# Kernel tuning notes

Hardware: AMD Instinct MI355X
Metric: run time of the kernel (lower is better)

## Reference

```python
import math
import jax, jax.numpy as jnp
import numpy as np

NUM_CLASSES = 80
CONF_THR = 0.05
IOU_THR = 0.5
MAX_PER_CLASS = 100
MAX_DET = 100
PRE_NMS_K = 200  # per-class candidates kept before greedy NMS (>= max_per_class)
BOX_VAR = np.array([0.1, 0.1, 0.2, 0.2], np.float32)
IMG_H, IMG_W = 640, 640
BATCH = 8


def _anchor_dims():
    ratios = [0.5, 1.0, 2.0]
    scales = [2.0 ** x for x in (0.0, 1.0 / 3.0, 2.0 / 3.0)]
    dims_all = []
    for area in [32.0 ** 2, 64.0 ** 2, 128.0 ** 2, 256.0 ** 2, 512.0 ** 2]:
        dims = []
        for r in ratios:  # ratio-major, scale-minor (matches AnchorBox._compute_dims)
            h = math.sqrt(area / r)
            w = area / h
            for s in scales:
                dims.append([s * w, s * h])
        dims_all.append(np.array(dims, np.float32))  # [9, 2]
    return dims_all


def get_anchors(H, W):
    """Anchors in [cx, cy, w, h], shape [total_anchors, 4] (static, numpy)."""
    strides = [8, 16, 32, 64, 128]
    out = []
    for stride, dims in zip(strides, _anchor_dims()):
        fh, fw = math.ceil(H / stride), math.ceil(W / stride)
        rx = (np.arange(fw, dtype=np.float32) + 0.5) * stride
        ry = (np.arange(fh, dtype=np.float32) + 0.5) * stride
        cx, cy = np.meshgrid(rx, ry)  # each [fh, fw], 'xy' indexing like tf.meshgrid
        centers = np.broadcast_to(np.stack([cx, cy], -1)[:, :, None, :], (fh, fw, 9, 2))
        d = np.broadcast_to(dims[None, None], (fh, fw, 9, 2))
        out.append(np.concatenate([centers, d], -1).reshape(-1, 4))
    return jnp.asarray(np.concatenate(out, 0))


def decode_boxes(anchors, box_pred):
    """Apply variance scaling + anchor offsets, return corner boxes."""
    b = box_pred * jnp.asarray(BOX_VAR)
    xy = b[..., :2] * anchors[..., 2:] + anchors[..., :2]
    wh = jnp.exp(b[..., 2:]) * anchors[..., 2:]
    return jnp.concatenate([xy - wh * 0.5, xy + wh * 0.5], axis=-1)


def pairwise_iou(b):
    lt = jnp.maximum(b[:, None, :2], b[None, :, :2])
    rb = jnp.minimum(b[:, None, 2:], b[None, :, 2:])
    wh = jnp.maximum(rb - lt, 0.0)
    inter = wh[..., 0] * wh[..., 1]
    area = (b[:, 2] - b[:, 0]) * (b[:, 3] - b[:, 1])
    return inter / (area[:, None] + area[None, :] - inter + 1e-8)


def nms_one_class(boxes, scores):
    """Greedy NMS over top PRE_NMS_K candidates for one class."""
    sc, idx = jax.lax.top_k(scores, PRE_NMS_K)
    bb = boxes[idx]  # [K, 4]
    valid = sc > CONF_THR
    iou = jax.lax.stop_gradient(pairwise_iou(bb))  # [K, K]
    ar = jnp.arange(PRE_NMS_K)

    def body(i, keep):
        supp = keep[i] & (iou[i] > IOU_THR) & (ar > i)
        return keep & ~supp

    keep = jax.lax.fori_loop(0, PRE_NMS_K, body, valid)
    sc = jnp.where(keep, sc, 0.0)
    sc2, j = jax.lax.top_k(sc, MAX_PER_CLASS)
    bb2 = jnp.where((sc2 > 0.0)[:, None], bb[j], 0.0)
    return bb2, sc2


def detect_one_image(boxes, cls_scores):
    """boxes [A,4] shared across classes, cls_scores [A,C]."""
    cb, cs = jax.vmap(nms_one_class, in_axes=(None, 1))(boxes, cls_scores)  # [C,100,4],[C,100]
    cls_id = jnp.broadcast_to(
        jnp.arange(NUM_CLASSES, dtype=jnp.float32)[:, None], cs.shape
    )
    flat_s = cs.reshape(-1)
    flat_b = cb.reshape(-1, 4)
    flat_c = cls_id.reshape(-1)
    s, i = jax.lax.top_k(flat_s, MAX_DET)
    b = jnp.where((s > 0.0)[:, None], flat_b[i], 0.0)
    c = jnp.where(s > 0.0, flat_c[i], 0.0)
    n = jnp.sum(s > 0.0).astype(jnp.int32)
    return b, s, c, n


def setup_inputs() -> dict:
    key = jax.random.key(0)
    k1, _ = jax.random.split(key)
    images = jnp.zeros((BATCH, IMG_H, IMG_W, 3), jnp.float32)  # only shape is used
    num_anchors = 76725  # 640x640 image -> (6400+1600+400+100+25)*9
    predictions = jax.random.normal(k1, (BATCH, num_anchors, 4 + NUM_CLASSES), jnp.float32)
    return {"images": images, "predictions": predictions}


def reference(images, predictions):
    H, W = images.shape[1], images.shape[2]
    anchors = get_anchors(H, W)  # [A, 4]
    box_pred = predictions[:, :, :4]
    cls_pred = jax.nn.sigmoid(predictions[:, :, 4:])  # [B, A, C]
    boxes = decode_boxes(anchors[None], box_pred)  # [B, A, 4]
    nmsed_boxes, nmsed_scores, nmsed_classes, valid = jax.vmap(detect_one_image)(
        boxes, cls_pred
    )
    return nmsed_boxes, nmsed_scores, nmsed_classes, valid
```

## Files before the change

### kernel.cpp

```cpp
#include <hip/hip_runtime.h>
#include <stdint.h>

typedef unsigned long long u64;
typedef unsigned int u32;
typedef unsigned char u8;

#define NB 8
#define NA 76725
#define NC 80
#define NCH 84
#define PRE_K 200
#define MAXPC 100
#define MAXDET 100
#define F4_PER_IMG (NA * 21u)

#define T0 0.93f
#define XCUT 2.58f
#define BLKX 256
#define SPAN (BLKX * 256u)
#define NSTEP 24
#define LCAP 24
#define CAP2 512
#define CAPF 2048


__device__ __forceinline__ float sigmoid_ref(float x) {
    return 1.0f / (1.0f + expf(-x));
}

__device__ void decode_box(float4 d, int a, float4* box, float* areaOut) {
    int lvl, off, fw, stride;
    if (a < 57600)      { lvl = 0; off = 0;     fw = 80; stride = 8;   }
    else if (a < 72000) { lvl = 1; off = 57600; fw = 40; stride = 16;  }
    else if (a < 75600) { lvl = 2; off = 72000; fw = 20; stride = 32;  }
    else if (a < 76500) { lvl = 3; off = 75600; fw = 10; stride = 64;  }
    else                { lvl = 4; off = 76500; fw = 5;  stride = 128; }
    int idx  = a - off;
    int k    = idx % 9;
    int cell = idx / 9;
    int row = cell / fw, col = cell - row * fw;
    float cx = __fmul_rn((float)col + 0.5f, (float)stride);
    float cy = __fmul_rn((float)row + 0.5f, (float)stride);
    int ri = k / 3, si = k - ri * 3;
    double r    = (ri == 0) ? 0.5 : ((ri == 1) ? 1.0 : 2.0);
    double side = (double)(32 << lvl);
    double area = side * side;
    double h = sqrt(area / r);
    double w = area / h;
    double s = exp2((double)si / 3.0);
    float aw = (float)(s * w);
    float ah = (float)(s * h);
    float b0 = __fmul_rn(d.x, 0.1f);
    float b1 = __fmul_rn(d.y, 0.1f);
    float b2 = __fmul_rn(d.z, 0.2f);
    float b3 = __fmul_rn(d.w, 0.2f);
    float ux = __fadd_rn(__fmul_rn(b0, aw), cx);
    float uy = __fadd_rn(__fmul_rn(b1, ah), cy);
    float wx = __fmul_rn(expf(b2), aw);
    float wy = __fmul_rn(expf(b3), ah);
    float hx = __fmul_rn(wx, 0.5f);
    float hy = __fmul_rn(wy, 0.5f);
    float x1 = __fsub_rn(ux, hx), y1 = __fsub_rn(uy, hy);
    float x2 = __fadd_rn(ux, hx), y2 = __fadd_rn(uy, hy);
    *box = make_float4(x1, y1, x2, y2);
    *areaOut = __fmul_rn(__fsub_rn(x2, x1), __fsub_rn(y2, y1));
}

__device__ __forceinline__ void bitonic_desc(u64* keys, u32 n) {
    for (u32 k = 2; k <= n; k <<= 1) {
        for (u32 j = k >> 1; j > 0; j >>= 1) {
            for (u32 i = threadIdx.x; i < n; i += blockDim.x) {
                u32 ixj = i ^ j;
                if (ixj > i) {
                    u64 x = keys[i], y = keys[ixj];
                    if (((i & k) == 0u) ? (x < y) : (x > y)) {
                        keys[i] = y; keys[ixj] = x;
                    }
                }
            }
            __syncthreads();
        }
    }
}


__device__ __forceinline__ void scan4(float4 v, u32 idx,
                                      u32* lhist, u64 (*llist)[LCAP]) {
    u32 a  = idx / 21u;
    u32 c4 = idx - a * 21u;
    if (c4 == 0u) return;
    float m = fmaxf(fmaxf(v.x, v.y), fmaxf(v.z, v.w));
    if (m <= XCUT) return;
    u32 cb = c4 * 4u - 4u;
    float vv[4] = {v.x, v.y, v.z, v.w};
#pragma unroll
    for (int q = 0; q < 4; ++q) {
        if (vv[q] > XCUT) {
            float sig = sigmoid_ref(vv[q]);
            if (sig > T0) {
                u32 c = cb + (u32)q;
                u64 key = ((u64)__float_as_uint(sig) << 32) | (u64)(~a);
                u32 p = atomicAdd(&lhist[c], 1u);
                if (p < LCAP) llist[c][p] = key;
            }
        }
    }
}

__global__ __launch_bounds__(256, 4) void k_scan(const float4* __restrict__ p4,
                                                 u64* __restrict__ seg,
                                                 u32* __restrict__ cntT) {
    __shared__ u32 lhist[NC];
    __shared__ u64 llist[NC][LCAP];
    u32 b = blockIdx.y, x = blockIdx.x;
    for (u32 c = threadIdx.x; c < NC; c += 256u) lhist[c] = 0u;
    __syncthreads();

    const float4* base = p4 + (u64)b * F4_PER_IMG;
    u32 i0 = x * 256u + threadIdx.x;
#pragma unroll 1
    for (int s = 0; s < NSTEP; s += 4) {
        u32 ia = i0 + (u32)s * SPAN;
        float4 v0 = base[ia];
        float4 v1 = base[ia + SPAN];
        float4 v2 = base[ia + 2u * SPAN];
        float4 v3 = base[ia + 3u * SPAN];
        scan4(v0, ia,            lhist, llist);
        scan4(v1, ia + SPAN,     lhist, llist);
        scan4(v2, ia + 2u*SPAN,  lhist, llist);
        scan4(v3, ia + 3u*SPAN,  lhist, llist);
    }
    {
        u32 it = i0 + (u32)NSTEP * SPAN;
        if (it < F4_PER_IMG) scan4(base[it], it, lhist, llist);
    }
    __syncthreads();

    if (threadIdx.x < NC) {
        u32 c = threadIdx.x;
        u32 n = lhist[c];
        u32 m = n < LCAP ? n : (u32)LCAP;
        u64* o = seg + ((u64)(b * NC + c) * BLKX + x) * LCAP;
        for (u32 j = 0; j < m; ++j) o[j] = llist[c][j];
        cntT[(b * NC + c) * BLKX + x] = n;
    }
}


__global__ __launch_bounds__(256) void k_nms(const float* __restrict__ pred,
                                             const u64* __restrict__ seg,
                                             const u32* __restrict__ cntT,
                                             float* __restrict__ sc2,
                                             float* __restrict__ bb2) {
    int bc = blockIdx.x;
    int b = bc / NC, c = bc % NC;
    __shared__ u64 keys[CAP2];
    __shared__ u32 gc[BLKX];
    __shared__ u32 gflag;
    __shared__ u32 gtot;
    __shared__ float4 box[PRE_K];
    __shared__ float area[PRE_K];
    __shared__ u32 suppT[PRE_K][7];
    __shared__ u32 validw[7];
    __shared__ u32 keepw[7];
    __shared__ u32 nkeep[7];
    __shared__ u32 chg;
    __shared__ u64 red[256];

    if (threadIdx.x == 0) gflag = 0u;
    __syncthreads();

    u32 m_c = 0;
    {
        u32 n = cntT[(u64)bc * BLKX + threadIdx.x];
        if (n > (u32)LCAP) atomicOr(&gflag, 1u);
        m_c = n < LCAP ? n : (u32)LCAP;
        gc[threadIdx.x] = m_c;
    }
    __syncthreads();
    for (u32 d = 1; d < BLKX; d <<= 1) {
        u32 v = 0;
        if (threadIdx.x >= d) v = gc[threadIdx.x - d];
        __syncthreads();
        gc[threadIdx.x] += v;
        __syncthreads();
    }
    if (threadIdx.x == 0) gtot = gc[BLKX - 1];
    __syncthreads();
    u32 total = gtot;
    bool repaired = (gflag != 0u) || (total < (u32)PRE_K) || (total > (u32)CAP2);

    if (!repaired) {
        {
            u32 dst = gc[threadIdx.x] - m_c;
            const u64* src = seg + ((u64)bc * BLKX + threadIdx.x) * LCAP;
            for (u32 j = 0; j < m_c; ++j) keys[dst + j] = src[j];
        }
        for (u32 i = threadIdx.x; i < CAP2; i += blockDim.x)
            if (i >= total) keys[i] = 0ull;
        __syncthreads();
        bitonic_desc(keys, CAP2);
    } else {
        u64 cur = ~0ull;
        for (int k = 0; k < PRE_K; ++k) {
            u64 loc = 0;
            for (int a = threadIdx.x; a < NA; a += blockDim.x) {
                float xx = pred[((long)b * NA + a) * NCH + 4 + c];
                float sg = sigmoid_ref(xx);
                u64 key  = ((u64)__float_as_uint(sg) << 32) | (u64)(~(u32)a);
                if (key < cur && key > loc) loc = key;
            }
            red[threadIdx.x] = loc;
            __syncthreads();
            for (int s = 128; s > 0; s >>= 1) {
                if (threadIdx.x < (u32)s) {
                    if (red[threadIdx.x + s] > red[threadIdx.x])
                        red[threadIdx.x] = red[threadIdx.x + s];
                }
                __syncthreads();
            }
            cur = red[0];
            if (threadIdx.x == 0) keys[k] = cur;
            __syncthreads();
        }
        for (u32 i = PRE_K + threadIdx.x; i < CAP2; i += blockDim.x) keys[i] = 0ull;
        __syncthreads();
    }

    for (int i = threadIdx.x; i < PRE_K * 7; i += blockDim.x) suppT[i / 7][i % 7] = 0u;
    if (threadIdx.x < 7) validw[threadIdx.x] = 0u;
    __syncthreads();

    if (threadIdx.x < PRE_K) {
        int r   = threadIdx.x;
        u64 key = keys[r];
        float sig = __uint_as_float((u32)(key >> 32));
        int a = (int)(~(u32)key);
        float4 bx = make_float4(0.f, 0.f, 0.f, 0.f);
        float ar = 0.f;
        if (sig > 0.05f) {
            float4 dd = *(const float4*)(pred + ((long)b * NA + a) * NCH);
            decode_box(dd, a, &bx, &ar);
            atomicOr(&validw[r >> 5], 1u << (r & 31));
        }
        box[r] = bx; area[r] = ar;
    }
    __syncthreads();

    for (int p = threadIdx.x; p < PRE_K * PRE_K; p += blockDim.x) {
        int i  = p / PRE_K;
        int jx = p - i * PRE_K;
        if (jx > i) {
            float4 bi = box[i], bj = box[jx];
            float ltx = fmaxf(bi.x, bj.x), lty = fmaxf(bi.y, bj.y);
            float rbx = fminf(bi.z, bj.z), rby = fminf(bi.w, bj.w);
            float wx = fmaxf(__fsub_rn(rbx, ltx), 0.f);
            float wy = fmaxf(__fsub_rn(rby, lty), 0.f);
            float inter = __fmul_rn(wx, wy);
            float den = __fadd_rn(__fsub_rn(__fadd_rn(area[i], area[jx]), inter), 1e-8f);
            float iou = __fdiv_rn(inter, den);
            if (iou > 0.5f) atomicOr(&suppT[jx][i >> 5], 1u << (i & 31));
        }
    }
    __syncthreads();
    if (threadIdx.x < 7) keepw[threadIdx.x] = validw[threadIdx.x];
    __syncthreads();

    for (int t = 0; t < PRE_K; ++t) {
        if (threadIdx.x < 7) nkeep[threadIdx.x] = 0u;
        if (threadIdx.x == 0) chg = 0u;
        __syncthreads();
        if (threadIdx.x < PRE_K) {
            int j = threadIdx.x;
            u32 sup = 0;
#pragma unroll
            for (int w = 0; w < 7; ++w) sup |= keepw[w] & suppT[j][w];
            u32 ob = (keepw[j >> 5] >> (j & 31)) & 1u;
            u32 vb = (validw[j >> 5] >> (j & 31)) & 1u;
            u32 nb = vb & (sup == 0u ? 1u : 0u);
            if (nb) atomicOr(&nkeep[j >> 5], 1u << (j & 31));
            if (nb != ob) chg = 1u;
        }
        __syncthreads();
        if (threadIdx.x < 7) keepw[threadIdx.x] = nkeep[threadIdx.x];
        __syncthreads();
        if (chg == 0u) break;
    }

    int kept = 0;
#pragma unroll
    for (int w = 0; w < 7; ++w) kept += __popc(keepw[w]);
    if (kept > MAXPC) kept = MAXPC;

    if (threadIdx.x >= (u32)kept && threadIdx.x < MAXPC) {
        int pos = threadIdx.x;
        sc2[bc * MAXPC + pos] = 0.f;
        float* o = bb2 + ((long)bc * MAXPC + pos) * 4;
        o[0] = 0.f; o[1] = 0.f; o[2] = 0.f; o[3] = 0.f;
    }
    if (threadIdx.x < PRE_K) {
        int r = threadIdx.x;
        if ((keepw[r >> 5] >> (r & 31)) & 1u) {
            int pos = 0;
            for (int w = 0; w < (r >> 5); ++w) pos += __popc(keepw[w]);
            pos += __popc(keepw[r >> 5] & ((1u << (r & 31)) - 1u));
            if (pos < MAXPC) {
                u64 key = keys[r];
                float sig = __uint_as_float((u32)(key >> 32));
                sc2[bc * MAXPC + pos] = sig;
                float4 bx = box[r];
                float* o = bb2 + ((long)bc * MAXPC + pos) * 4;
                o[0] = bx.x; o[1] = bx.y; o[2] = bx.z; o[3] = bx.w;
            }
        }
    }
}


__global__ __launch_bounds__(1024) void k_final(const float* __restrict__ sc2,
                                                const float* __restrict__ bb2,
                                                float* __restrict__ out) {
    int b = blockIdx.x;
    __shared__ u32 hist[256];
    __shared__ u32 sfx[256];
    __shared__ u64 keys[CAPF];
    __shared__ u32 cnt_s;
    __shared__ int t_s;
    __shared__ u64 red[1024];

    for (int i = threadIdx.x; i < 256; i += blockDim.x) hist[i] = 0u;
    if (threadIdx.x == 0) { cnt_s = 0u; t_s = 0; }
    __syncthreads();

    const float* s_b = sc2 + b * (NC * MAXPC);
    for (int f = threadIdx.x; f < NC * MAXPC; f += blockDim.x) {
        float s = s_b[f];
        if (s > 0.f) {
            int bin = (int)(s * 256.f); if (bin > 255) bin = 255;
            atomicAdd(&hist[bin], 1u);
        }
    }
    __syncthreads();

    if (threadIdx.x < 256) sfx[threadIdx.x] = hist[threadIdx.x];
    __syncthreads();
    for (u32 d = 1; d < 256u; d <<= 1) {
        u32 v = 0;
        if (threadIdx.x < 256u && threadIdx.x + d < 256u) v = sfx[threadIdx.x + d];
        __syncthreads();
        if (threadIdx.x < 256u) sfx[threadIdx.x] += v;
        __syncthreads();
    }
    if (threadIdx.x < 256) {
        bool ge = sfx[threadIdx.x] >= (u32)MAXDET;
        bool nlt = (threadIdx.x == 255) || (sfx[threadIdx.x + 1] < (u32)MAXDET);
        if (ge && nlt) t_s = (int)threadIdx.x;
    }
    __syncthreads();
    int t = t_s;

    for (int f = threadIdx.x; f < NC * MAXPC; f += blockDim.x) {
        float s = s_b[f];
        if (s > 0.f) {
            int bin = (int)(s * 256.f); if (bin > 255) bin = 255;
            if (bin >= t) {
                u32 pos = atomicAdd(&cnt_s, 1u);
                if (pos < CAPF)
                    keys[pos] = ((u64)__float_as_uint(s) << 32) | (u64)(~(u32)f);
            }
        }
    }
    __syncthreads();
    u32 g = cnt_s;

    if (g <= (u32)CAPF) {
        u32 n = (g <= 1024u) ? 1024u : (u32)CAPF;
        for (u32 i = threadIdx.x; i < n; i += blockDim.x)
            if (i >= g) keys[i] = 0ull;
        __syncthreads();
        bitonic_desc(keys, n);
    } else {
        __syncthreads();
        u64 cur = ~0ull;
        for (int k = 0; k < MAXDET; ++k) {
            u64 loc = 0;
            for (int f = threadIdx.x; f < NC * MAXPC; f += blockDim.x) {
                float s = s_b[f];
                if (s > 0.f) {
                    u64 key = ((u64)__float_as_uint(s) << 32) | (u64)(~(u32)f);
                    if (key < cur && key > loc) loc = key;
                }
            }
            red[threadIdx.x] = loc;
            __syncthreads();
            for (int st = 512; st > 0; st >>= 1) {
                if (threadIdx.x < (u32)st) {
                    if (red[threadIdx.x + st] > red[threadIdx.x])
                        red[threadIdx.x] = red[threadIdx.x + st];
                }
                __syncthreads();
            }
            cur = red[0];
            if (threadIdx.x == 0) keys[k] = cur;
            __syncthreads();
        }
        if (threadIdx.x == 0) {
            u32 nv = 0;
            for (int r = 0; r < MAXDET; ++r) if (keys[r] != 0ull) ++nv;
            cnt_s = nv;
        }
        __syncthreads();
        g = cnt_s;
    }

    if (threadIdx.x < MAXDET) {
        int r = threadIdx.x;
        u64 key = keys[r];
        u32 hi = (u32)(key >> 32);
        float s = 0.f, cf = 0.f;
        float bx0 = 0.f, bx1 = 0.f, bx2 = 0.f, bx3 = 0.f;
        if (hi != 0u) {
            s = __uint_as_float(hi);
            int f = (int)(~(u32)key);
            int c = f / MAXPC, jj = f - c * MAXPC;
            const float* bsrc = bb2 + ((long)(b * NC + c) * MAXPC + jj) * 4;
            bx0 = bsrc[0]; bx1 = bsrc[1]; bx2 = bsrc[2]; bx3 = bsrc[3];
            cf = (float)c;
        }
        float* ob = out + ((long)b * MAXDET + r) * 4;
        ob[0] = bx0; ob[1] = bx1; ob[2] = bx2; ob[3] = bx3;
        out[NB * MAXDET * 4 + b * MAXDET + r] = s;
        out[NB * MAXDET * 4 + NB * MAXDET + b * MAXDET + r] = cf;
    }
    if (threadIdx.x == 0) {
        u32 nv = g < (u32)MAXDET ? g : (u32)MAXDET;
        out[NB * MAXDET * 4 + 2 * NB * MAXDET + b] = (float)nv;
    }
}


extern "C" void kernel_launch(void* const* d_in, const int* in_sizes, int n_in,
                              void* d_out, int out_size, void* d_ws, size_t ws_size,
                              hipStream_t stream) {
    const float* pred = (const float*)d_in[1];
    if (n_in >= 2 && in_sizes[0] == NB * NA * NCH) pred = (const float*)d_in[0];

    char* ws = (char*)d_ws;
    const long BCN = (long)NB * NC;
    u64* seg   = (u64*)ws;
    char* p    = ws + BCN * BLKX * LCAP * 8;
    u32* cntT  = (u32*)p;            p += BCN * BLKX * 4;
    float* sc2 = (float*)p;          p += BCN * MAXPC * 4;
    float* bb2 = (float*)p;

    k_scan <<<dim3(BLKX, NB), 256, 0, stream>>>((const float4*)pred, seg, cntT);
    k_nms  <<<dim3(NB * NC),  256, 0, stream>>>(pred, seg, cntT, sc2, bb2);
    k_final<<<dim3(NB),      1024, 0, stream>>>(sc2, bb2, (float*)d_out);
}
```

Before: 123.2 us.

## Replace bitonic sorts with rank-by-count selection and wave-level NMS bitmasks

Both the per-class NMS kernel and the final top-k kernel drop the barrier-heavy bitonic sort. In its place, each thread computes the rank of its key by counting larger keys and scatters only the top entries. The NMS kernel now uses wavefront shuffles and ballots for the prefix sum, overflow flag, valid mask and keep-mask iteration. Each thread keeps its own suppression row in registers instead of a shared matrix filled with atomics. This cuts many __syncthreads and shared atomics, but the rank pass is O(n²) reads of shared memory per block, up to 2048 keys in the final kernel.

New measurement: 111.0 us. 9.9% less time.

```diff
diff --git a/kernel.cpp b/kernel.cpp
--- a/kernel.cpp
+++ b/kernel.cpp
@@ -66,23 +66,6 @@
     *areaOut = __fmul_rn(__fsub_rn(x2, x1), __fsub_rn(y2, y1));
 }
 
-__device__ __forceinline__ void bitonic_desc(u64* keys, u32 n) {
-    for (u32 k = 2; k <= n; k <<= 1) {
-        for (u32 j = k >> 1; j > 0; j >>= 1) {
-            for (u32 i = threadIdx.x; i < n; i += blockDim.x) {
-                u32 ixj = i ^ j;
-                if (ixj > i) {
-                    u64 x = keys[i], y = keys[ixj];
-                    if (((i & k) == 0u) ? (x < y) : (x > y)) {
-                        keys[i] = y; keys[ixj] = x;
-                    }
-                }
-            }
-            __syncthreads();
-        }
-    }
-}
-
 
 __device__ __forceinline__ void scan4(float4 v, u32 idx,
                                       u32* lhist, u64 (*llist)[LCAP]) {
@@ -155,136 +138,148 @@
     int bc = blockIdx.x;
     int b = bc / NC, c = bc % NC;
     __shared__ u64 keys[CAP2];
-    __shared__ u32 gc[BLKX];
-    __shared__ u32 gflag;
-    __shared__ u32 gtot;
+    __shared__ u64 sorted[PRE_K];
+    __shared__ u32 wsum[4];
+    __shared__ u32 oflow[4];
     __shared__ float4 box[PRE_K];
     __shared__ float area[PRE_K];
-    __shared__ u32 suppT[PRE_K][7];
-    __shared__ u32 validw[7];
-    __shared__ u32 keepw[7];
-    __shared__ u32 nkeep[7];
+    __shared__ u32 validw[8];
+    __shared__ u32 keepw[8];
     __shared__ u32 chg;
     __shared__ u64 red[256];
 
-    if (threadIdx.x == 0) gflag = 0u;
-    __syncthreads();
-
-    u32 m_c = 0;
-    {
-        u32 n = cntT[(u64)bc * BLKX + threadIdx.x];
-        if (n > (u32)LCAP) atomicOr(&gflag, 1u);
-        m_c = n < LCAP ? n : (u32)LCAP;
-        gc[threadIdx.x] = m_c;
-    }
-    __syncthreads();
-    for (u32 d = 1; d < BLKX; d <<= 1) {
-        u32 v = 0;
-        if (threadIdx.x >= d) v = gc[threadIdx.x - d];
-        __syncthreads();
-        gc[threadIdx.x] += v;
-        __syncthreads();
-    }
-    if (threadIdx.x == 0) gtot = gc[BLKX - 1];
-    __syncthreads();
-    u32 total = gtot;
-    bool repaired = (gflag != 0u) || (total < (u32)PRE_K) || (total > (u32)CAP2);
+    u32 tid = threadIdx.x, lane = tid & 63u, wv = tid >> 6;
+
+    u32 n_raw = cntT[(u64)bc * BLKX + tid];
+    u32 m_c = n_raw < LCAP ? n_raw : (u32)LCAP;
+    u32 v = m_c;
+#pragma unroll
+    for (u32 d = 1; d < 64u; d <<= 1) {
+        u32 t = __shfl_up(v, d, 64);
+        if (lane >= d) v += t;
+    }
+    u64 ob = __ballot(n_raw > (u32)LCAP);
+    if (lane == 63u) wsum[wv] = v;
+    if (lane == 0u)  oflow[wv] = (ob != 0ull) ? 1u : 0u;
+    __syncthreads();
+    u32 off = 0;
+    for (u32 w = 0; w < wv; ++w) off += wsum[w];
+    u32 inc = v + off;
+    u32 total = wsum[0] + wsum[1] + wsum[2] + wsum[3];
+    bool over = (oflow[0] | oflow[1] | oflow[2] | oflow[3]) != 0u;
+    bool repaired = over || (total < (u32)PRE_K) || (total > (u32)CAP2);
 
     if (!repaired) {
-        {
-            u32 dst = gc[threadIdx.x] - m_c;
-            const u64* src = seg + ((u64)bc * BLKX + threadIdx.x) * LCAP;
-            for (u32 j = 0; j < m_c; ++j) keys[dst + j] = src[j];
-        }
-        for (u32 i = threadIdx.x; i < CAP2; i += blockDim.x)
-            if (i >= total) keys[i] = 0ull;
-        __syncthreads();
-        bitonic_desc(keys, CAP2);
+        u32 dst = inc - m_c;
+        const u64* src = seg + ((u64)bc * BLKX + tid) * LCAP;
+        for (u32 j = 0; j < m_c; ++j) keys[dst + j] = src[j];
+        __syncthreads();
+        u64 ka = (tid < total) ? keys[tid] : 0ull;
+        u64 kb = (tid + 256u < total) ? keys[tid + 256u] : 0ull;
+        u32 ra = 0, rb = 0;
+        for (u32 j = 0; j < total; ++j) {
+            u64 kj = keys[j];
+            ra += (kj > ka) ? 1u : 0u;
+            rb += (kj > kb) ? 1u : 0u;
+        }
+        if (tid < total && ra < (u32)PRE_K) sorted[ra] = ka;
+        if (tid + 256u < total && rb < (u32)PRE_K) sorted[rb] = kb;
+        __syncthreads();
     } else {
         u64 cur = ~0ull;
         for (int k = 0; k < PRE_K; ++k) {
             u64 loc = 0;
-            for (int a = threadIdx.x; a < NA; a += blockDim.x) {
+            for (int a = tid; a < NA; a += 256) {
                 float xx = pred[((long)b * NA + a) * NCH + 4 + c];
                 float sg = sigmoid_ref(xx);
                 u64 key  = ((u64)__float_as_uint(sg) << 32) | (u64)(~(u32)a);
                 if (key < cur && key > loc) loc = key;
             }
-            red[threadIdx.x] = loc;
+            red[tid] = loc;
             __syncthreads();
             for (int s = 128; s > 0; s >>= 1) {
-                if (threadIdx.x < (u32)s) {
-                    if (red[threadIdx.x + s] > red[threadIdx.x])
-                        red[threadIdx.x] = red[threadIdx.x + s];
+                if (tid < (u32)s) {
+                    if (red[tid + s] > red[tid]) red[tid] = red[tid + s];
                 }
                 __syncthreads();
             }
             cur = red[0];
-            if (threadIdx.x == 0) keys[k] = cur;
+            if (tid == 0) sorted[k] = cur;
             __syncthreads();
         }
-        for (u32 i = PRE_K + threadIdx.x; i < CAP2; i += blockDim.x) keys[i] = 0ull;
-        __syncthreads();
-    }
-
-    for (int i = threadIdx.x; i < PRE_K * 7; i += blockDim.x) suppT[i / 7][i % 7] = 0u;
-    if (threadIdx.x < 7) validw[threadIdx.x] = 0u;
-    __syncthreads();
-
-    if (threadIdx.x < PRE_K) {
-        int r   = threadIdx.x;
-        u64 key = keys[r];
+    }
+
+    bool val = false;
+    float4 mybox = make_float4(0.f, 0.f, 0.f, 0.f);
+    float myarea = 0.f;
+    if (tid < (u32)PRE_K) {
+        u64 key = sorted[tid];
         float sig = __uint_as_float((u32)(key >> 32));
         int a = (int)(~(u32)key);
-        float4 bx = make_float4(0.f, 0.f, 0.f, 0.f);
-        float ar = 0.f;
         if (sig > 0.05f) {
             float4 dd = *(const float4*)(pred + ((long)b * NA + a) * NCH);
-            decode_box(dd, a, &bx, &ar);
-            atomicOr(&validw[r >> 5], 1u << (r & 31));
-        }
-        box[r] = bx; area[r] = ar;
-    }
-    __syncthreads();
-
-    for (int p = threadIdx.x; p < PRE_K * PRE_K; p += blockDim.x) {
-        int i  = p / PRE_K;
-        int jx = p - i * PRE_K;
-        if (jx > i) {
-            float4 bi = box[i], bj = box[jx];
-            float ltx = fmaxf(bi.x, bj.x), lty = fmaxf(bi.y, bj.y);
-            float rbx = fminf(bi.z, bj.z), rby = fminf(bi.w, bj.w);
-            float wx = fmaxf(__fsub_rn(rbx, ltx), 0.f);
-            float wy = fmaxf(__fsub_rn(rby, lty), 0.f);
-            float inter = __fmul_rn(wx, wy);
-            float den = __fadd_rn(__fsub_rn(__fadd_rn(area[i], area[jx]), inter), 1e-8f);
-            float iou = __fdiv_rn(inter, den);
-            if (iou > 0.5f) atomicOr(&suppT[jx][i >> 5], 1u << (i & 31));
-        }
-    }
-    __syncthreads();
-    if (threadIdx.x < 7) keepw[threadIdx.x] = validw[threadIdx.x];
+            decode_box(dd, a, &mybox, &myarea);
+            val = true;
+        }
+        box[tid] = mybox; area[tid] = myarea;
+    }
+    u64 vbal = __ballot(val);
+    if (lane == 0u) {
+        validw[2u * wv]      = (u32)vbal;
+        validw[2u * wv + 1u] = (u32)(vbal >> 32);
+        keepw[2u * wv]       = (u32)vbal;
+        keepw[2u * wv + 1u]  = (u32)(vbal >> 32);
+    }
+    __syncthreads();
+
+    u32 rsup[7];
+#pragma unroll
+    for (int w = 0; w < 7; ++w) {
+        u32 m = 0;
+        if (val && (u32)(w * 32) < tid) {
+            for (int ii = 0; ii < 32; ++ii) {
+                int i = w * 32 + ii;
+                if ((u32)i < tid) {
+                    float4 bi = box[i];
+                    float ai = area[i];
+                    float ltx = fmaxf(bi.x, mybox.x), lty = fmaxf(bi.y, mybox.y);
+                    float rbx = fminf(bi.z, mybox.z), rby = fminf(bi.w, mybox.w);
+                    float wx = fmaxf(__fsub_rn(rbx, ltx), 0.f);
+                    float wy = fmaxf(__fsub_rn(rby, lty), 0.f);
+                    float inter = __fmul_rn(wx, wy);
+                    float den = __fadd_rn(__fsub_rn(__fadd_rn(ai, myarea), inter), 1e-8f);
+                    float iou = __fdiv_rn(inter, den);
+                    if (iou > 0.5f) m |= 1u << ii;
+                }
+            }
+        }
+        rsup[w] = m;
+    }
     __syncthreads();
 
     for (int t = 0; t < PRE_K; ++t) {
-        if (threadIdx.x < 7) nkeep[threadIdx.x] = 0u;
-        if (threadIdx.x == 0) chg = 0u;
-        __syncthreads();
-        if (threadIdx.x < PRE_K) {
-            int j = threadIdx.x;
-            u32 sup = 0;
-#pragma unroll
-            for (int w = 0; w < 7; ++w) sup |= keepw[w] & suppT[j][w];
-            u32 ob = (keepw[j >> 5] >> (j & 31)) & 1u;
-            u32 vb = (validw[j >> 5] >> (j & 31)) & 1u;
-            u32 nb = vb & (sup == 0u ? 1u : 0u);
-            if (nb) atomicOr(&nkeep[j >> 5], 1u << (j & 31));
-            if (nb != ob) chg = 1u;
-        }
-        __syncthreads();
-        if (threadIdx.x < 7) keepw[threadIdx.x] = nkeep[threadIdx.x];
-        __syncthreads();
-        if (chg == 0u) break;
+        if (tid == 0) chg = 0u;
+        __syncthreads();
+        u32 k0 = keepw[0], k1 = keepw[1], k2 = keepw[2], k3 = keepw[3];
+        u32 k4 = keepw[4], k5 = keepw[5], k6 = keepw[6];
+        bool nb = false;
+        if (val) {
+            u32 sup = (k0 & rsup[0]) | (k1 & rsup[1]) | (k2 & rsup[2]) |
+                      (k3 & rsup[3]) | (k4 & rsup[4]) | (k5 & rsup[5]) |
+                      (k6 & rsup[6]);
+            nb = (sup == 0u);
+        }
+        u64 bal = __ballot(nb);
+        u64 oldk = ((u64)keepw[2u * wv + 1u] << 32) | (u64)keepw[2u * wv];
+        if (lane == 0u) {
+            keepw[2u * wv]      = (u32)bal;
+            keepw[2u * wv + 1u] = (u32)(bal >> 32);
+            if (bal != oldk) chg = 1u;
+        }
+        __syncthreads();
+        u32 cflag = chg;
+        __syncthreads();
+        if (cflag == 0u) break;
     }
 
     int kept = 0;
@@ -292,25 +287,24 @@
     for (int w = 0; w < 7; ++w) kept += __popc(keepw[w]);
     if (kept > MAXPC) kept = MAXPC;
 
-    if (threadIdx.x >= (u32)kept && threadIdx.x < MAXPC) {
-        int pos = threadIdx.x;
+    if (tid >= (u32)kept && tid < (u32)MAXPC) {
+        int pos = tid;
         sc2[bc * MAXPC + pos] = 0.f;
         float* o = bb2 + ((long)bc * MAXPC + pos) * 4;
         o[0] = 0.f; o[1] = 0.f; o[2] = 0.f; o[3] = 0.f;
     }
-    if (threadIdx.x < PRE_K) {
-        int r = threadIdx.x;
+    if (tid < (u32)PRE_K) {
+        int r = tid;
         if ((keepw[r >> 5] >> (r & 31)) & 1u) {
             int pos = 0;
             for (int w = 0; w < (r >> 5); ++w) pos += __popc(keepw[w]);
             pos += __popc(keepw[r >> 5] & ((1u << (r & 31)) - 1u));
             if (pos < MAXPC) {
-                u64 key = keys[r];
+                u64 key = sorted[r];
                 float sig = __uint_as_float((u32)(key >> 32));
                 sc2[bc * MAXPC + pos] = sig;
-                float4 bx = box[r];
                 float* o = bb2 + ((long)bc * MAXPC + pos) * 4;
-                o[0] = bx.x; o[1] = bx.y; o[2] = bx.z; o[3] = bx.w;
+                o[0] = mybox.x; o[1] = mybox.y; o[2] = mybox.z; o[3] = mybox.w;
             }
         }
     }
@@ -324,11 +318,13 @@
     __shared__ u32 hist[256];
     __shared__ u32 sfx[256];
     __shared__ u64 keys[CAPF];
+    __shared__ u64 top[128];
     __shared__ u32 cnt_s;
     __shared__ int t_s;
     __shared__ u64 red[1024];
 
     for (int i = threadIdx.x; i < 256; i += blockDim.x) hist[i] = 0u;
+    if (threadIdx.x < 128) top[threadIdx.x] = 0ull;
     if (threadIdx.x == 0) { cnt_s = 0u; t_s = 0; }
     __syncthreads();
 
@@ -374,13 +370,18 @@
     u32 g = cnt_s;
 
     if (g <= (u32)CAPF) {
-        u32 n = (g <= 1024u) ? 1024u : (u32)CAPF;
-        for (u32 i = threadIdx.x; i < n; i += blockDim.x)
-            if (i >= g) keys[i] = 0ull;
-        __syncthreads();
-        bitonic_desc(keys, n);
+        u64 ka = (threadIdx.x < g) ? keys[threadIdx.x] : 0ull;
+        u64 kb = (threadIdx.x + 1024u < g) ? keys[threadIdx.x + 1024u] : 0ull;
+        u32 ra = 0, rb = 0;
+        for (u32 j = 0; j < g; ++j) {
+            u64 kj = keys[j];
+            ra += (kj > ka) ? 1u : 0u;
+            rb += (kj > kb) ? 1u : 0u;
+        }
+        if (threadIdx.x < g && ra < (u32)MAXDET) top[ra] = ka;
+        if (threadIdx.x + 1024u < g && rb < (u32)MAXDET) top[rb] = kb;
+        __syncthreads();
     } else {
-        __syncthreads();
         u64 cur = ~0ull;
         for (int k = 0; k < MAXDET; ++k) {
             u64 loc = 0;
@@ -401,12 +402,12 @@
                 __syncthreads();
             }
             cur = red[0];
-            if (threadIdx.x == 0) keys[k] = cur;
+            if (threadIdx.x == 0) top[k] = cur;
             __syncthreads();
         }
         if (threadIdx.x == 0) {
             u32 nv = 0;
-            for (int r = 0; r < MAXDET; ++r) if (keys[r] != 0ull) ++nv;
+            for (int r = 0; r < MAXDET; ++r) if (top[r] != 0ull) ++nv;
             cnt_s = nv;
         }
         __syncthreads();
@@ -415,7 +416,7 @@
 
     if (threadIdx.x < MAXDET) {
         int r = threadIdx.x;
-        u64 key = keys[r];
+        u64 key = top[r];
         u32 hi = (u32)(key >> 32);
         float s = 0.f, cf = 0.f;
         float bx0 = 0.f, bx1 = 0.f, bx2 = 0.f, bx3 = 0.f;
```
